# Performance work log

Measured on AMD Instinct MI355X. Metric: run time of the kernel, lower is better.

Reference implementation:

```python
import jax, jax.numpy as jnp
import numpy as np

NUM_ITER = 2
MIN_FILTER_REG = 1e-5
NUM_BINS = 10
BIN_DISP = 0.5
BG_MASK_VAL = 0.0
STEPLEN_REG = 0.0


def apply_filter(feat, filt):
    # feat: [1, S, C, H, W], filt: [S, NF, C, fh, fw] -> scores [1, S, NF, H, W]
    _, S, C, H, W = feat.shape
    NF, fh, fw = filt.shape[1], filt.shape[3], filt.shape[4]
    out = jax.lax.conv_general_dilated(
        feat.reshape(1, S * C, H, W),
        filt.reshape(S * NF, C, fh, fw),
        window_strides=(1, 1),
        padding=[(fh // 2, fh // 2), (fw // 2, fw // 2)],
        feature_group_count=S)
    return out.reshape(1, S, NF, H, W)


def apply_feat_transpose(feat, residuals, filt_shape):
    # gradient of apply_filter w.r.t. the filter (conv transpose on weights)
    zero = jnp.zeros(filt_shape, feat.dtype)
    _, vjp = jax.vjp(lambda w: apply_filter(feat, w), zero)
    return vjp(residuals)[0]


def distance_map(dH, dW, cy, cx):
    # pytracking DistanceMap: soft bin assignment of radial distance, [NUM_BINS, dH, dW]
    d0 = jnp.arange(dH, dtype=jnp.float32) - cy
    d1 = jnp.arange(dW, dtype=jnp.float32) - cx
    dist = jnp.sqrt(d0[:, None] ** 2 + d1[None, :] ** 2)
    bin_diff = dist[None] / BIN_DISP - jnp.arange(NUM_BINS, dtype=jnp.float32)[:, None, None]
    main = jax.nn.relu(1.0 - jnp.abs(bin_diff[:-1]))
    last = jnp.clip(1.0 + bin_diff[-1:], 0.0, 1.0)
    return jnp.concatenate([main, last], axis=0)


def unfold_map(full_map, H, W):
    # equivalent of F.unfold(...).view(H,W,H,W).flip((2,3)).permute(2,3,0,1)
    # map[i*W+j, y, x] = full_map[H-1-i+y, W-1-j+x]
    yy = (H - 1) - jnp.arange(H)[:, None] + jnp.arange(H)[None, :]  # [i, y]
    xx = (W - 1) - jnp.arange(W)[:, None] + jnp.arange(W)[None, :]  # [j, x]
    m = full_map[yy[:, None, :, None], xx[None, :, None, :]]        # [i, j, y, x]
    return m.reshape(1, 1, H * W, H, W)


def setup_inputs() -> dict:
    key = jax.random.key(0)
    k1, k2 = jax.random.split(key)
    S, C, H, W, fsz = 8, 256, 23, 23, 3
    NF = H * W
    filt = jax.random.normal(k1, (S, NF, C, fsz, fsz), jnp.float32) * 0.01
    feat = jax.random.normal(k2, (1, S, C, H, W), jnp.float32)
    # label_map_predictor init: gauss(sigma=1.0) over bin centers, min-subtracted
    d = jnp.arange(NUM_BINS, dtype=jnp.float32) * BIN_DISP
    g = jnp.exp(-0.5 * (d / 1.0) ** 2)
    w_label = g - g.min()
    w_spatial = jnp.ones((NUM_BINS,), jnp.float32)
    log_step_length = jnp.zeros((), jnp.float32)       # log(1.0)
    filter_reg = jnp.asarray(0.01, jnp.float32)
    return {"filter": filt, "feat": feat, "w_label": w_label, "w_spatial": w_spatial,
            "log_step_length": log_step_length, "filter_reg": filter_reg}


def reference(filter, feat, w_label, w_spatial, log_step_length, filter_reg):
    f = filter
    _, S, C, H, W = feat.shape
    NF = f.shape[1]
    dH, dW = 2 * H - 1, 2 * W - 1
    bins = distance_map(dH, dW, dH // 2, dW // 2)                 # [B, dH, dW]
    label_full = jnp.einsum('b,bhw->hw', w_label, bins)           # 1x1 conv
    spatial_full = jnp.einsum('b,bhw->hw', w_spatial, bins)
    label_map = unfold_map(label_full, H, W)                      # [1,1,NF,H,W]
    spatial_weight = unfold_map(spatial_full, H, W)
    tm = (1.0 - BG_MASK_VAL) * jnp.eye(NF, dtype=f.dtype).reshape(1, 1, NF, H, W) + BG_MASK_VAL
    step_length = jnp.exp(log_step_length)
    reg_weight = jnp.maximum(filter_reg * filter_reg, MIN_FILTER_REG ** 2)

    for _ in range(NUM_ITER):
        scores = apply_filter(feat, f)                            # [1,S,NF,H,W]
        # LeakyReluPar activation parameterized by target mask
        scores_act = (1.0 - tm) * 0.5 * jnp.abs(scores) + (1.0 + tm) * 0.5 * scores
        score_mask = (1.0 - tm) * 0.5 * jnp.sign(jax.lax.stop_gradient(scores)) + (1.0 + tm) * 0.5
        loss_residuals = spatial_weight * (scores_act - label_map)
        mapped_residuals = score_mask * (spatial_weight * loss_residuals)
        filter_grad = apply_feat_transpose(feat, mapped_residuals, f.shape) + reg_weight * f
        scores_grad = apply_filter(feat, filter_grad)
        scores_grad = spatial_weight * (score_mask * scores_grad)
        alpha_num = (filter_grad * filter_grad).reshape(S, NF, -1).sum(-1)   # [S, NF]
        alpha_den = jnp.maximum(
            (scores_grad * scores_grad).reshape(S, NF, -1).sum(-1) + reg_weight * alpha_num, 1e-8)
        alpha_den = alpha_den + STEPLEN_REG * alpha_num
        alpha = alpha_num / alpha_den
        f = f - step_length * alpha.reshape(S, NF, 1, 1, 1) * filter_grad
    return f
```

## Files before the change

kernel.cpp:

```cpp
#include <hip/hip_runtime.h>
#include <math.h>

#define NF   529
#define K9   2304
#define NP   544
#define DMAP 45

typedef unsigned short ush;
typedef unsigned int u32;
typedef __bf16 bf8_t __attribute__((ext_vector_type(8)));
typedef float f4_t __attribute__((ext_vector_type(4)));
typedef ush ush8 __attribute__((ext_vector_type(8)));


__device__ __forceinline__ ush f2bf(float f) {
  union { float f; u32 u; } v; v.f = f;
  u32 r = v.u + 0x7fffu + ((v.u >> 16) & 1u);
  return (ush)(r >> 16);
}
__device__ __forceinline__ float bf2f(ush h) {
  union { u32 u; float f; } v; v.u = ((u32)h) << 16;
  return v.f;
}
__device__ __forceinline__ void async16(const void* g, void* l) {
  __builtin_amdgcn_global_load_lds((const __attribute__((address_space(1))) u32*)g,
                                   (__attribute__((address_space(3))) u32*)l, 16, 0, 0);
}

__global__ void build_maps(const float* __restrict__ wl, const float* __restrict__ wsp,
                           float* __restrict__ labelF, float* __restrict__ spatialF) {
  int idx = blockIdx.x * blockDim.x + threadIdx.x;
  if (idx >= DMAP * DMAP) return;
  int h = idx / DMAP, w = idx % DMAP;
  float dy = (float)(h - 22), dx = (float)(w - 22);
  float dist = sqrtf(dy * dy + dx * dx);
  float lab = 0.f, sp = 0.f;
#pragma unroll
  for (int b = 0; b < 9; ++b) {
    float bd = dist * 2.f - (float)b;
    float wt = fmaxf(0.f, 1.f - fabsf(bd));
    lab += wl[b] * wt;
    sp  += wsp[b] * wt;
  }
  float bd = dist * 2.f - 9.f;
  float wt = fminf(fmaxf(1.f + bd, 0.f), 1.f);
  lab += wl[9] * wt;
  sp  += wsp[9] * wt;
  labelF[idx] = lab;
  spatialF[idx] = sp;
}

__global__ void convert_f(const float* __restrict__ filt, float* __restrict__ F,
                          ush* __restrict__ Fhl) {
  int g = blockIdx.x * 256 + threadIdx.x;
  int row = g / 288;
  int kk = (g - row * 288) * 8;
  int s = row / NF, m = row - s * NF;
  const float4* fp = (const float4*)(filt + (size_t)row * K9 + kk);
  float4 a = fp[0], b = fp[1];
  float4* Fp = (float4*)(F + (size_t)row * K9 + kk);
  Fp[0] = a; Fp[1] = b;
  float vv[8] = {a.x, a.y, a.z, a.w, b.x, b.y, b.z, b.w};
  ush8 h, lo;
#pragma unroll
  for (int i = 0; i < 8; ++i) {
    ush hh = f2bf(vv[i]);
    h[i] = hh;
    lo[i] = f2bf(vv[i] - bf2f(hh));
  }
  size_t o = ((size_t)s * 576 + m) * (2 * K9) + (kk >> 5) * 64 + (kk & 31);
  *(ush8*)(Fhl + o) = h;
  *(ush8*)(Fhl + o + 32) = lo;
}

__global__ void im2col_pack(const float* __restrict__ feat,
                            ush* __restrict__ Xbhl, ush* __restrict__ XThl) {
  __shared__ float T[64][65];
  int s = blockIdx.z, k0 = blockIdx.y * 64, yx0 = blockIdx.x * 64;
  int t = threadIdx.x;
  int r = t >> 2, c4 = (t & 3) * 16;
  int k = k0 + r;
  int ck = k / 9, j = k - ck * 9;
  int dy = j / 3 - 1, dx = j - (j / 3) * 3 - 1;
  const float* fb = feat + ((size_t)s * 256 + ck) * 529;
  float v[16];
#pragma unroll
  for (int i = 0; i < 16; ++i) {
    int yx = yx0 + c4 + i;
    float vv = 0.f;
    if (yx < NF) {
      int yy = yx / 23;
      int y = yy + dy, x = yx - yy * 23 + dx;
      if (y >= 0 && y < 23 && x >= 0 && x < 23) vv = fb[y * 23 + x];
    }
    v[i] = vv;
    T[r][c4 + i] = vv;
  }
  int c0 = yx0 + c4;
  if (c0 < NP) {
    size_t o = ((size_t)s * K9 + k) * (2 * NP) + (c0 >> 5) * 64 + (c0 & 31);
    ush8 h[2], lo[2];
#pragma unroll
    for (int gg = 0; gg < 2; ++gg)
#pragma unroll
      for (int i = 0; i < 8; ++i) {
        float vv = v[gg * 8 + i];
        ush hh = f2bf(vv);
        h[gg][i] = hh;
        lo[gg][i] = f2bf(vv - bf2f(hh));
      }
    *(ush8*)(Xbhl + o) = h[0];
    *(ush8*)(Xbhl + o + 8) = h[1];
    *(ush8*)(Xbhl + o + 32) = lo[0];
    *(ush8*)(Xbhl + o + 40) = lo[1];
  }
  __syncthreads();
  int kc = k0 + c4;
  size_t o2 = ((size_t)s * 640 + yx0 + r) * (2 * K9) + (kc >> 5) * 64 + (kc & 31);
  ush8 h2[2], l2[2];
#pragma unroll
  for (int gg = 0; gg < 2; ++gg)
#pragma unroll
    for (int i = 0; i < 8; ++i) {
      float vv = T[c4 + gg * 8 + i][r];
      ush hh = f2bf(vv);
      h2[gg][i] = hh;
      l2[gg][i] = f2bf(vv - bf2f(hh));
    }
  *(ush8*)(XThl + o2) = h2[0];
  *(ush8*)(XThl + o2 + 8) = h2[1];
  *(ush8*)(XThl + o2 + 32) = l2[0];
  *(ush8*)(XThl + o2 + 40) = l2[1];
}

template <int KTOT, int ASPL, int BSPL, int MODE, int SKC, int CH, int BPG, int GX>
__launch_bounds__(256, 6)
__global__ void gemm128(const ush* __restrict__ Ahl, const ush* __restrict__ Bhl,
                        float* __restrict__ Cp,
                        const float* __restrict__ F, const float* __restrict__ frp,
                        ush* __restrict__ FGhl, float* __restrict__ numb,
                        const int arows) {
  __shared__ ush As[ASPL][128 * 32];
  __shared__ ush Bs[BSPL][64 * 32];

  const int tid = threadIdx.x;
  const int w = tid >> 6, l = tid & 63;
  const int wm = w & 1, wn = w >> 1;
  const int q = l >> 4, c = l & 15;

  const int xcd = blockIdx.x & 7;
  const int t = blockIdx.x >> 3;
  const int g = xcd + 8 * (t / BPG);
  const int j = t % BPG;
  const int s = g / SKC, sk = g % SKC;
  const int x = j % GX, y = j / GX;
  const int m0 = x * 128, n0 = y * 64;

  const ush* A0 = Ahl + (size_t)s * arows * (2 * KTOT);
  const ush* B0 = Bhl + (size_t)s * ((MODE == 2) ? K9 : 640) * (2 * KTOT);

  const int srow = w * 16 + (l >> 2);
  const int scol = (l & 3) * 8;
  const int ssw  = ((((l & 3) - (l >> 3)) & 3)) * 8;
  const int rb   = tid >> 2;
  const int sb   = (tid & 3) * 8;
  const int sswb = (((tid & 3) - (tid >> 3)) & 3) * 8;

  auto stage = [&](int ch) {
    const int k2 = (sk * CH + ch) * 64;
#pragma unroll
    for (int i = 0; i < 2; ++i) {
      size_t ro = (size_t)(m0 + i * 64 + srow) * (2 * KTOT) + k2 + ssw;
      async16(A0 + ro, &As[0][(i * 64 + srow) * 32 + scol]);
      if (ASPL == 2) async16(A0 + ro + 32, &As[1][(i * 64 + srow) * 32 + scol]);
    }
    {
      size_t ro = (size_t)(n0 + rb) * (2 * KTOT) + k2 + sswb;
      async16(B0 + ro, &Bs[0][rb * 32 + sb]);
      if (BSPL == 2) async16(B0 + ro + 32, &Bs[1][rb * 32 + sb]);
    }
  };

  f4_t acc[4][2];
#pragma unroll
  for (int i = 0; i < 4; ++i)
#pragma unroll
    for (int jj = 0; jj < 2; ++jj) acc[i][jj] = (f4_t){0.f, 0.f, 0.f, 0.f};

  const int slotA = (((q + (c >> 1)) & 3)) * 8;

  stage(0);

  for (int ch = 0; ch < CH; ++ch) {
    __syncthreads();

    bf8_t av[ASPL][4], bv[BSPL][2];
#pragma unroll
    for (int pp = 0; pp < ASPL; ++pp)
#pragma unroll
      for (int ti = 0; ti < 4; ++ti)
        av[pp][ti] = *(const bf8_t*)&As[pp][(wm * 64 + ti * 16 + c) * 32 + slotA];
#pragma unroll
    for (int pp = 0; pp < BSPL; ++pp)
#pragma unroll
      for (int tj = 0; tj < 2; ++tj)
        bv[pp][tj] = *(const bf8_t*)&Bs[pp][(wn * 32 + tj * 16 + c) * 32 + slotA];

    __syncthreads();
    if (ch + 1 < CH) stage(ch + 1);

#pragma unroll
    for (int ti = 0; ti < 4; ++ti)
#pragma unroll
      for (int tj = 0; tj < 2; ++tj) {
        acc[ti][tj] = __builtin_amdgcn_mfma_f32_16x16x32_bf16(av[0][ti], bv[0][tj], acc[ti][tj], 0, 0, 0);
        if (ASPL == 2)
          acc[ti][tj] = __builtin_amdgcn_mfma_f32_16x16x32_bf16(av[1][ti], bv[0][tj], acc[ti][tj], 0, 0, 0);
        if (BSPL == 2)
          acc[ti][tj] = __builtin_amdgcn_mfma_f32_16x16x32_bf16(av[0][ti], bv[1][tj], acc[ti][tj], 0, 0, 0);
      }
  }

  if (MODE == 0) {
    float* C = Cp + (size_t)(sk * 8 + s) * 640 * 640;
#pragma unroll
    for (int ti = 0; ti < 4; ++ti)
#pragma unroll
      for (int tj = 0; tj < 2; ++tj)
#pragma unroll
        for (int r = 0; r < 4; ++r) {
          int m = m0 + wm * 64 + ti * 16 + q * 4 + r;
          int n = n0 + wn * 32 + tj * 16 + c;
          __builtin_nontemporal_store(acc[ti][tj][r], &C[(size_t)m * 640 + n]);
        }
  } else {
    float reg = fmaxf(frp[0] * frp[0], 1e-10f);
#pragma unroll
    for (int ti = 0; ti < 4; ++ti) {
      float ps[4] = {0.f, 0.f, 0.f, 0.f};
      int mb = m0 + wm * 64 + ti * 16 + q * 4;
#pragma unroll
      for (int tj = 0; tj < 2; ++tj) {
        int n = n0 + wn * 32 + tj * 16 + c;
#pragma unroll
        for (int r = 0; r < 4; ++r) {
          int m = mb + r;
          if (m < NF) {
            float v = acc[ti][tj][r] + reg * F[((size_t)s * NF + m) * K9 + n];
            size_t o = ((size_t)s * 576 + m) * (2 * K9) + ((n >> 5) * 64) + (n & 31);
            ush h = f2bf(v);
            FGhl[o] = h;
            FGhl[o + 32] = f2bf(v - bf2f(h));
            ps[r] += v * v;
          }
        }
      }
#pragma unroll
      for (int r = 0; r < 4; ++r) {
        float pp = ps[r];
        pp += __shfl_xor(pp, 1); pp += __shfl_xor(pp, 2);
        pp += __shfl_xor(pp, 4); pp += __shfl_xor(pp, 8);
        if (c == 0 && (mb + r) < NF) atomicAdd(&numb[s * NF + mb + r], pp);
      }
    }
  }
}

__global__ void reduce_epi1(const float* __restrict__ Cp,
                            const float* __restrict__ labelF, const float* __restrict__ spatialF,
                            ush* __restrict__ Rbhl, ush* __restrict__ Mb) {
  int row = blockIdx.x;
  int s = row / NF, m = row - s * NF;
  int a = m / 23, b = m - a * 23;
  const size_t sp = (size_t)8 * 640 * 640;
  const float* C = Cp + ((size_t)s * 640 + m) * 640;
  for (int n = threadIdx.x; n < NF; n += 256) {
    float v = __builtin_nontemporal_load(&C[n]) +
              __builtin_nontemporal_load(&C[sp + n]) +
              __builtin_nontemporal_load(&C[2 * sp + n]) +
              __builtin_nontemporal_load(&C[3 * sp + n]);
    int yy = n / 23, xx = n - yy * 23;
    int idx = (22 + yy - a) * DMAP + (22 + xx - b);
    float sw = spatialF[idx], lm = labelF[idx];
    float sa, msk;
    if (m == n) { sa = v; msk = 1.f; }
    else {
      sa = 0.5f * fabsf(v) + 0.5f * v;
      msk = (v > 0.f) ? 1.f : ((v < 0.f) ? 0.f : 0.5f);
    }
    float rv = msk * sw * sw * (sa - lm);
    size_t o = ((size_t)s * 640 + m) * (2 * NP) + ((n >> 5) * 64) + (n & 31);
    ush h = f2bf(rv);
    Rbhl[o] = h;
    Rbhl[o + 32] = f2bf(rv - bf2f(h));
    Mb[((size_t)s * NF + m) * NP + n] = f2bf(msk);
  }
}

__global__ void reduce_epi3(const float* __restrict__ Cp,
                            const float* __restrict__ spatialF, const ush* __restrict__ Mb,
                            float* __restrict__ denb) {
  int row = blockIdx.x;
  int s = row / NF, m = row - s * NF;
  int a = m / 23, b = m - a * 23;
  const size_t sp = (size_t)8 * 640 * 640;
  const float* C = Cp + ((size_t)s * 640 + m) * 640;
  float ss = 0.f;
  for (int n = threadIdx.x; n < NF; n += 256) {
    float v = __builtin_nontemporal_load(&C[n]) +
              __builtin_nontemporal_load(&C[sp + n]) +
              __builtin_nontemporal_load(&C[2 * sp + n]) +
              __builtin_nontemporal_load(&C[3 * sp + n]);
    int yy = n / 23, xx = n - yy * 23;
    int idx = (22 + yy - a) * DMAP + (22 + xx - b);
    float sw = spatialF[idx];
    float msk = bf2f(Mb[((size_t)s * NF + m) * NP + n]);
    float z = sw * msk * v;
    ss += z * z;
  }
  __shared__ float red[256];
  red[threadIdx.x] = ss; __syncthreads();
  for (int st = 128; st > 0; st >>= 1) {
    if (threadIdx.x < st) red[threadIdx.x] += red[threadIdx.x + st];
    __syncthreads();
  }
  if (threadIdx.x == 0) denb[row] = red[0];
}

__global__ void update_f(float* __restrict__ F, const ush* __restrict__ FGhl,
                         const float* __restrict__ numb, const float* __restrict__ denb,
                         const float* __restrict__ lsp, const float* __restrict__ frp,
                         ush* __restrict__ Fhl) {
  int g = blockIdx.x * 256 + threadIdx.x;
  int row = g / 288;
  int kk = (g - row * 288) * 8;
  int s = row / NF, m = row - s * NF;
  float reg = fmaxf(frp[0] * frp[0], 1e-10f);
  float nm = numb[row], dn = denb[row];
  float alpha = nm / fmaxf(dn + reg * nm, 1e-8f);
  float sa = expf(lsp[0]) * alpha;
  size_t o = ((size_t)s * 576 + m) * (2 * K9) + (kk >> 5) * 64 + (kk & 31);
  ush8 gh = *(const ush8*)(FGhl + o);
  ush8 gl = *(const ush8*)(FGhl + o + 32);
  float4* Fp = (float4*)(F + (size_t)row * K9 + kk);
  float4 a = Fp[0], b = Fp[1];
  float f[8] = {a.x, a.y, a.z, a.w, b.x, b.y, b.z, b.w};
  ush8 h, lo;
#pragma unroll
  for (int i = 0; i < 8; ++i) {
    f[i] -= sa * (bf2f(gh[i]) + bf2f(gl[i]));
    ush hh = f2bf(f[i]);
    h[i] = hh;
    lo[i] = f2bf(f[i] - bf2f(hh));
  }
  Fp[0] = (float4){f[0], f[1], f[2], f[3]};
  Fp[1] = (float4){f[4], f[5], f[6], f[7]};
  *(ush8*)(Fhl + o) = h;
  *(ush8*)(Fhl + o + 32) = lo;
}

extern "C" void kernel_launch(void* const* d_in, const int* in_sizes, int n_in,
                              void* d_out, int out_size, void* d_ws, size_t ws_size,
                              hipStream_t stream) {
  const float* filt = (const float*)d_in[0];
  const float* feat = (const float*)d_in[1];
  const float* wl   = (const float*)d_in[2];
  const float* wsp  = (const float*)d_in[3];
  const float* lsp  = (const float*)d_in[4];
  const float* frp  = (const float*)d_in[5];
  float* F = (float*)d_out;

  float* fb       = (float*)d_ws;
  float* labelF   = fb;
  float* spatialF = fb + 2048;
  float* numden   = fb + 4096;
  ush* cur = (ush*)(fb + 4096 + 4 * 4240);

  const size_t szF  = (size_t)8 * 576 * (2 * K9);
  const size_t szXT = (size_t)8 * 640 * (2 * K9);
  const size_t szXb = (size_t)8 * K9 * (2 * NP);
  const size_t szRb = (size_t)8 * 640 * (2 * NP);
  const size_t szMb = (size_t)8 * NF * NP;

  ush* Fhl  = cur;           cur += szF;
  ush* FGhl = cur;           cur += szF;
  ush* XThl = cur;           cur += szXT;
  ush* Xbhl = cur;           cur += szXb;
  ush* Rbhl = cur;           cur += szRb;
  ush* Mb   = cur;           cur += szMb;
  float* Cp = (float*)((((size_t)cur) + 15) & ~(size_t)15);

  build_maps<<<8, 256, 0, stream>>>(wl, wsp, labelF, spatialF);
  hipMemsetAsync(numden, 0, 4 * 4240 * sizeof(float), stream);
  convert_f<<<4761, 256, 0, stream>>>(filt, F, Fhl);
  im2col_pack<<<dim3(10, 36, 8), 256, 0, stream>>>(feat, Xbhl, XThl);

  for (int it = 0; it < 2; ++it) {
    float* numb = numden + it * 2 * 4240;
    float* denb = numb + 4240;
    gemm128<K9, 2, 2, 0, 4, 18, 50, 5><<<1600, 256, 0, stream>>>(
        Fhl, XThl, Cp, nullptr, nullptr, nullptr, nullptr, 576);
    reduce_epi1<<<8 * NF, 256, 0, stream>>>(Cp, labelF, spatialF, Rbhl, Mb);
    gemm128<NP, 2, 2, 2, 1, 17, 180, 5><<<1440, 256, 0, stream>>>(
        Rbhl, Xbhl, nullptr, F, frp, FGhl, numb, 640);
    gemm128<K9, 1, 1, 0, 4, 18, 50, 5><<<1600, 256, 0, stream>>>(
        FGhl, XThl, Cp, nullptr, nullptr, nullptr, nullptr, 576);
    reduce_epi3<<<8 * NF, 256, 0, stream>>>(Cp, spatialF, Mb, denb);
    update_f<<<4761, 256, 0, stream>>>(F, FGhl, numb, denb, lsp, frp, Fhl);
  }
}
```

Measured before the change: 523.2 us.

## Double-buffer GEMM LDS tiles with two-deep async prefetch

```diff
diff --git a/kernel.cpp b/kernel.cpp
--- a/kernel.cpp
+++ b/kernel.cpp
@@ -134,14 +134,14 @@
 }
 
 template <int KTOT, int ASPL, int BSPL, int MODE, int SKC, int CH, int BPG, int GX>
-__launch_bounds__(256, 6)
+__launch_bounds__(256, (ASPL + BSPL >= 4) ? 3 : 6)
 __global__ void gemm128(const ush* __restrict__ Ahl, const ush* __restrict__ Bhl,
                         float* __restrict__ Cp,
                         const float* __restrict__ F, const float* __restrict__ frp,
                         ush* __restrict__ FGhl, float* __restrict__ numb,
                         const int arows) {
-  __shared__ ush As[ASPL][128 * 32];
-  __shared__ ush Bs[BSPL][64 * 32];
+  __shared__ ush As[2][ASPL][128 * 32];
+  __shared__ ush Bs[2][BSPL][64 * 32];
 
   const int tid = threadIdx.x;
   const int w = tid >> 6, l = tid & 63;
@@ -166,18 +166,18 @@
   const int sb   = (tid & 3) * 8;
   const int sswb = (((tid & 3) - (tid >> 3)) & 3) * 8;
 
-  auto stage = [&](int ch) {
+  auto stage = [&](int ch, int b) {
     const int k2 = (sk * CH + ch) * 64;
 #pragma unroll
     for (int i = 0; i < 2; ++i) {
       size_t ro = (size_t)(m0 + i * 64 + srow) * (2 * KTOT) + k2 + ssw;
-      async16(A0 + ro, &As[0][(i * 64 + srow) * 32 + scol]);
-      if (ASPL == 2) async16(A0 + ro + 32, &As[1][(i * 64 + srow) * 32 + scol]);
+      async16(A0 + ro, &As[b][0][(i * 64 + srow) * 32 + scol]);
+      if (ASPL == 2) async16(A0 + ro + 32, &As[b][1][(i * 64 + srow) * 32 + scol]);
     }
     {
       size_t ro = (size_t)(n0 + rb) * (2 * KTOT) + k2 + sswb;
-      async16(B0 + ro, &Bs[0][rb * 32 + sb]);
-      if (BSPL == 2) async16(B0 + ro + 32, &Bs[1][rb * 32 + sb]);
+      async16(B0 + ro, &Bs[b][0][rb * 32 + sb]);
+      if (BSPL == 2) async16(B0 + ro + 32, &Bs[b][1][rb * 32 + sb]);
     }
   };
 
@@ -189,25 +189,36 @@
 
   const int slotA = (((q + (c >> 1)) & 3)) * 8;
 
-  stage(0);
+  stage(0, 0);
+  stage(1, 1);
 
   for (int ch = 0; ch < CH; ++ch) {
-    __syncthreads();
+    const int cur = ch & 1;
+
+    if (ch + 1 < CH) {
+      if constexpr (2 * ASPL + BSPL == 6) asm volatile("s_waitcnt vmcnt(6)" ::: "memory");
+      else                                asm volatile("s_waitcnt vmcnt(3)" ::: "memory");
+    } else {
+      asm volatile("s_waitcnt vmcnt(0)" ::: "memory");
+    }
+    __builtin_amdgcn_s_barrier();
 
     bf8_t av[ASPL][4], bv[BSPL][2];
 #pragma unroll
     for (int pp = 0; pp < ASPL; ++pp)
 #pragma unroll
       for (int ti = 0; ti < 4; ++ti)
-        av[pp][ti] = *(const bf8_t*)&As[pp][(wm * 64 + ti * 16 + c) * 32 + slotA];
+        av[pp][ti] = *(const bf8_t*)&As[cur][pp][(wm * 64 + ti * 16 + c) * 32 + slotA];
 #pragma unroll
     for (int pp = 0; pp < BSPL; ++pp)
 #pragma unroll
       for (int tj = 0; tj < 2; ++tj)
-        bv[pp][tj] = *(const bf8_t*)&Bs[pp][(wn * 32 + tj * 16 + c) * 32 + slotA];
-
-    __syncthreads();
-    if (ch + 1 < CH) stage(ch + 1);
+        bv[pp][tj] = *(const bf8_t*)&Bs[cur][pp][(wn * 32 + tj * 16 + c) * 32 + slotA];
+
+    asm volatile("s_waitcnt lgkmcnt(0)" ::: "memory");
+    __builtin_amdgcn_sched_barrier(0);
+    __builtin_amdgcn_s_barrier();
+    if (ch + 2 < CH) stage(ch + 2, cur);
 
 #pragma unroll
     for (int ti = 0; ti < 4; ++ti)
```

Result: slower. 545.4 us (+4.2%).
